# Kernel tuning notes

Measured on AMD Instinct MI355X. Metric: run time of the kernel, lower is better.

Reference implementation:

```python
import jax, jax.numpy as jnp
import numpy as np

B, S, D_IN, UNITS = 4, 4096, 256, 64


def setup_inputs() -> dict:
    key = jax.random.key(0)
    ks = jax.random.split(key, 4)
    scale = 1.0 / np.sqrt(D_IN)
    return {
        "x": jax.random.normal(ks[0], (B, S, D_IN), dtype=jnp.float32),
        "Wq": jax.random.normal(ks[1], (D_IN, UNITS), dtype=jnp.float32) * scale,
        "bq": jnp.zeros((UNITS,), dtype=jnp.float32),
        "Wk": jax.random.normal(ks[2], (D_IN, UNITS), dtype=jnp.float32) * scale,
        "bk": jnp.zeros((UNITS,), dtype=jnp.float32),
        "Wv": jax.random.normal(ks[3], (D_IN, UNITS), dtype=jnp.float32) * scale,
        "bv": jnp.zeros((UNITS,), dtype=jnp.float32),
    }


def reference(x, Wq, bq, Wk, bk, Wv, bv):
    # Q/K/V projections: [B, S, D_IN] @ [D_IN, UNITS] -> [B, S, UNITS]
    q = jnp.einsum("bsd,du->bsu", x, Wq) + bq
    k = jnp.einsum("bsd,du->bsu", x, Wk) + bk
    v = jnp.einsum("bsd,du->bsu", x, Wv) + bv
    # Full [B, S, S] scores (the module materializes these - headroom target)
    sims = jnp.einsum("bsu,btu->bst", q, k) / np.sqrt(UNITS).astype(np.float32)
    attn = jax.nn.softmax(sims, axis=-1)
    out = jnp.einsum("bst,btu->bsu", attn, v)
    return out  # activation is None (linear)
```

## Files before the change

### kernel.cpp

```cpp
#include <hip/hip_runtime.h>
#include <hip/hip_bf16.h>

#define B_ 4
#define S_ 4096
#define D_ 256
#define U_ 64
#define NROWS (B_ * S_)
#define QSCALE 0.1803368801111244f

typedef __attribute__((ext_vector_type(8))) short short8;
typedef __attribute__((ext_vector_type(8))) float float8;
typedef __attribute__((ext_vector_type(4))) float floatx4;

__device__ inline short f2bf(float f) {
    union { __hip_bfloat16 h; short s; } u;
    u.h = __float2bfloat16(f);
    return u.s;
}
__device__ inline unsigned pk2bf(float a, float b) {
    unsigned ua = __float_as_uint(a) + 0x8000u;
    unsigned ub = __float_as_uint(b) + 0x8000u;
    return (ub & 0xFFFF0000u) | (ua >> 16);
}

__global__ void pack_w_kernel(const float* __restrict__ Wq,
                              const float* __restrict__ Wk,
                              const float* __restrict__ Wv,
                              short* __restrict__ wpack) {
    int tid = blockIdx.x * 256 + threadIdx.x;
    if (tid >= 3 * 16384) return;
    int p = tid >> 14, e = tid & 16383;
    const float* W = (p == 0) ? Wq : (p == 1) ? Wk : Wv;
    float w = W[e];
    int k = e >> 6, n = e & 63;
    int ks = k >> 5, hi = (k >> 3) & 3, j = k & 7;
    int l = hi * 16 + (n & 15), nc = n >> 4;
    wpack[p * 16384 + ((ks * 4 + nc) * 64 + l) * 8 + j] = f2bf(w);
}

__global__ __launch_bounds__(256) void qkv_proj_kernel(
    const float* __restrict__ x, const short* __restrict__ wpack,
    const float* __restrict__ bq, const float* __restrict__ bk,
    const float* __restrict__ bv,
    short* __restrict__ Q, short* __restrict__ Kpack, short* __restrict__ Vpack) {
    __shared__ __align__(16) short k_sh[64][72];
    __shared__ __align__(16) short vT_sh[64][72];
    const int wl    = threadIdx.x >> 6;
    const int lane  = threadIdx.x & 63;
    const int col16 = lane & 15, quad = lane >> 4;
    const int m0b = blockIdx.x * 64, m0 = m0b + wl * 16;

    floatx4 acc[3][4];
#pragma unroll
    for (int p = 0; p < 3; ++p)
#pragma unroll
        for (int nc = 0; nc < 4; ++nc) acc[p][nc] = (floatx4){0.f, 0.f, 0.f, 0.f};

    const float* xrow = x + (size_t)(m0 + col16) * D_ + quad * 8;
#pragma unroll
    for (int ks = 0; ks < 8; ++ks) {
        float8 af = *(const float8*)(xrow + ks * 32);
        short8 a;
#pragma unroll
        for (int j = 0; j < 8; ++j) a[j] = f2bf(af[j]);
#pragma unroll
        for (int p = 0; p < 3; ++p) {
#pragma unroll
            for (int nc = 0; nc < 4; ++nc) {
                short8 bfr = *(const short8*)(wpack +
                    ((size_t)((p * 8 + ks) * 4 + nc) * 64 + lane) * 8);
                acc[p][nc] = __builtin_amdgcn_mfma_f32_16x16x32_bf16(a, bfr, acc[p][nc], 0, 0, 0);
            }
        }
    }

#pragma unroll
    for (int nc = 0; nc < 4; ++nc) {
        float biasq = bq[nc * 16 + col16];
        float biask = bk[nc * 16 + col16];
        float biasv = bv[nc * 16 + col16];
#pragma unroll
        for (int r = 0; r < 4; ++r) {
            int row = m0 + quad * 4 + r;
            Q[(size_t)row * U_ + nc * 16 + col16] = f2bf((acc[0][nc][r] + biasq) * QSCALE);
            k_sh[wl * 16 + quad * 4 + r][nc * 16 + col16] = f2bf(acc[1][nc][r] + biask);
        }
        union { short s[4]; unsigned long long u; } pv;
#pragma unroll
        for (int r = 0; r < 4; ++r) pv.s[r] = f2bf(acc[2][nc][r] + biasv);
        *(unsigned long long*)&vT_sh[nc * 16 + col16][wl * 16 + quad * 4] = pv.u;
    }
    __syncthreads();

#pragma unroll
    for (int c2 = 0; c2 < 2; ++c2) {
        int combo = wl + c2 * 4;
        int ww = combo >> 2, t = (combo >> 1) & 1, h = combo & 1;
        int srow = ww * 32 + (col16 >> 2) * 8 + (col16 & 3) + 4 * t;
        short8 v = *(const short8*)&k_sh[srow][h * 32 + quad * 8];
        size_t gt = (size_t)blockIdx.x * 2 + ww;
        *(short8*)(Kpack + (gt * 4 + t * 2 + h) * 512 + lane * 8) = v;
    }
#pragma unroll
    for (int c2 = 0; c2 < 2; ++c2) {
        int combo = wl + c2 * 4;
        int ww = combo >> 2, nc = combo & 3;
        short8 v = *(const short8*)&vT_sh[nc * 16 + col16][ww * 32 + quad * 8];
        size_t gt = (size_t)blockIdx.x * 2 + ww;
        *(short8*)(Vpack + (gt * 4 + nc) * 512 + lane * 8) = v;
    }
}

__global__ __launch_bounds__(512) void attn_kernel(
    const short* __restrict__ Q, const short* __restrict__ Kpack,
    const short* __restrict__ Vpack, float* __restrict__ out) {
    __shared__ float o_sh[2][64][65];
    __shared__ float l_sh[8][4][16];

    const int b  = blockIdx.y;
    const int q0 = blockIdx.x * 64;
    const int kw = threadIdx.x >> 6;
    const int lane  = threadIdx.x & 63;
    const int col16 = lane & 15, quad = lane >> 4;

    const short* Qb = Q + (size_t)b * S_ * U_;

    short8 bQ[4][2];
#pragma unroll
    for (int qs = 0; qs < 4; ++qs) {
        const short* qrow = Qb + (size_t)(q0 + qs * 16 + col16) * U_ + quad * 8;
        bQ[qs][0] = *(const short8*)(qrow);
        bQ[qs][1] = *(const short8*)(qrow + 32);
    }

    floatx4 o[4][4];
#pragma unroll
    for (int qs = 0; qs < 4; ++qs)
#pragma unroll
        for (int nc = 0; nc < 4; ++nc) o[qs][nc] = (floatx4){0.f, 0.f, 0.f, 0.f};
    float l_i[4] = {0.f, 0.f, 0.f, 0.f};

    const short* kbase = Kpack + ((size_t)(b * 128 + kw * 16)) * 2048 + lane * 8;
    const short* vbase = Vpack + ((size_t)(b * 128 + kw * 16)) * 2048 + lane * 8;

    for (int it = 0; it < 16; ++it) {
        const short* kp = kbase + it * 2048;
        const short* vp = vbase + it * 2048;
        short8 ak[2][2];
#pragma unroll
        for (int t = 0; t < 2; ++t)
#pragma unroll
            for (int h = 0; h < 2; ++h)
                ak[t][h] = *(const short8*)(kp + (t * 2 + h) * 512);
        short8 av[4];
#pragma unroll
        for (int nc = 0; nc < 4; ++nc)
            av[nc] = *(const short8*)(vp + nc * 512);

#pragma unroll
        for (int qs = 0; qs < 4; ++qs) {
            floatx4 c[2];
#pragma unroll
            for (int t = 0; t < 2; ++t) {
                c[t] = __builtin_amdgcn_mfma_f32_16x16x32_bf16(ak[t][0], bQ[qs][0],
                          (floatx4){0.f, 0.f, 0.f, 0.f}, 0, 0, 0);
                c[t] = __builtin_amdgcn_mfma_f32_16x16x32_bf16(ak[t][1], bQ[qs][1], c[t], 0, 0, 0);
            }
            float p[8];
            float rs = 0.f;
#pragma unroll
            for (int t = 0; t < 2; ++t)
#pragma unroll
                for (int r = 0; r < 4; ++r) {
                    float e = exp2f(c[t][r]);
                    p[t * 4 + r] = e;
                    rs += e;
                }
            l_i[qs] += rs;
            union { short8 s; unsigned u[4]; } pb;
            pb.u[0] = pk2bf(p[0], p[1]);
            pb.u[1] = pk2bf(p[2], p[3]);
            pb.u[2] = pk2bf(p[4], p[5]);
            pb.u[3] = pk2bf(p[6], p[7]);
#pragma unroll
            for (int nc = 0; nc < 4; ++nc)
                o[qs][nc] = __builtin_amdgcn_mfma_f32_16x16x32_bf16(av[nc], pb.s, o[qs][nc], 0, 0, 0);
        }
    }

#pragma unroll
    for (int qs = 0; qs < 4; ++qs) {
        l_i[qs] += __shfl_xor(l_i[qs], 16, 64);
        l_i[qs] += __shfl_xor(l_i[qs], 32, 64);
    }
    if (quad == 0) {
#pragma unroll
        for (int qs = 0; qs < 4; ++qs) l_sh[kw][qs][col16] = l_i[qs];
    }

    if (kw < 2) {
#pragma unroll
        for (int qs = 0; qs < 4; ++qs)
#pragma unroll
            for (int nc = 0; nc < 4; ++nc)
#pragma unroll
                for (int r = 0; r < 4; ++r)
                    o_sh[kw][qs * 16 + col16][nc * 16 + quad * 4 + r] = o[qs][nc][r];
    }
    __syncthreads();
    if (kw == 2 || kw == 3) {
#pragma unroll
        for (int qs = 0; qs < 4; ++qs)
#pragma unroll
            for (int nc = 0; nc < 4; ++nc)
#pragma unroll
                for (int r = 0; r < 4; ++r)
                    o_sh[kw - 2][qs * 16 + col16][nc * 16 + quad * 4 + r] += o[qs][nc][r];
    }
    __syncthreads();
    if (kw == 4 || kw == 5) {
#pragma unroll
        for (int qs = 0; qs < 4; ++qs)
#pragma unroll
            for (int nc = 0; nc < 4; ++nc)
#pragma unroll
                for (int r = 0; r < 4; ++r)
                    o_sh[kw - 4][qs * 16 + col16][nc * 16 + quad * 4 + r] += o[qs][nc][r];
    }
    __syncthreads();
    if (kw >= 6) {
#pragma unroll
        for (int qs = 0; qs < 4; ++qs)
#pragma unroll
            for (int nc = 0; nc < 4; ++nc)
#pragma unroll
                for (int r = 0; r < 4; ++r)
                    o_sh[kw - 6][qs * 16 + col16][nc * 16 + quad * 4 + r] += o[qs][nc][r];
    }
    __syncthreads();
    for (int i = threadIdx.x; i < 64 * 64; i += 512) {
        int row = i >> 6, col = i & 63;
        int qs2 = row >> 4, c = row & 15;
        float lt = 0.f;
#pragma unroll
        for (int ww = 0; ww < 8; ++ww) lt += l_sh[ww][qs2][c];
        float s = o_sh[0][row][col] + o_sh[1][row][col];
        out[((size_t)b * S_ + q0 + row) * U_ + col] = s / lt;
    }
}

extern "C" void kernel_launch(void* const* d_in, const int* in_sizes, int n_in,
                              void* d_out, int out_size, void* d_ws, size_t ws_size,
                              hipStream_t stream) {
    const float* x  = (const float*)d_in[0];
    const float* Wq = (const float*)d_in[1];
    const float* bq = (const float*)d_in[2];
    const float* Wk = (const float*)d_in[3];
    const float* bk = (const float*)d_in[4];
    const float* Wv = (const float*)d_in[5];
    const float* bv = (const float*)d_in[6];
    float* out = (float*)d_out;

    short* Q     = (short*)d_ws;
    short* Kpack = Q + (size_t)NROWS * U_;
    short* Vpack = Kpack + (size_t)NROWS * U_;
    short* wpack = Vpack + (size_t)NROWS * U_;

    pack_w_kernel<<<192, 256, 0, stream>>>(Wq, Wk, Wv, wpack);
    qkv_proj_kernel<<<NROWS / 64, 256, 0, stream>>>(
        x, wpack, bq, bk, bv, Q, Kpack, Vpack);
    attn_kernel<<<dim3(S_ / 64, B_), 512, 0, stream>>>(Q, Kpack, Vpack, out);
}
```

Baseline: 120.7 us.

## Double-buffer K/V tile loads, use native exp2, and swizzle block order

The attention loop now prefetches the next K/V tile into a second register buffer while computing the current one, so global-load latency overlaps with MFMA and exp work. exp2f is replaced by the hardware exp2 builtin when the compiler provides it. The launch becomes a 1D grid of 256 blocks whose index is remapped so that neighbouring blocks handle different batches, which is meant to spread K/V reads of one batch across XCDs or caches. The extra buffer raises VGPR pressure, which could hurt occupancy at 512 threads.

```diff
diff --git a/kernel.cpp b/kernel.cpp
--- a/kernel.cpp
+++ b/kernel.cpp
@@ -21,6 +21,13 @@
     unsigned ua = __float_as_uint(a) + 0x8000u;
     unsigned ub = __float_as_uint(b) + 0x8000u;
     return (ub & 0xFFFF0000u) | (ua >> 16);
+}
+__device__ inline float fast_exp2(float x) {
+#if __has_builtin(__builtin_amdgcn_exp2f)
+    return __builtin_amdgcn_exp2f(x);
+#else
+    return exp2f(x);
+#endif
 }
 
 __global__ void pack_w_kernel(const float* __restrict__ Wq,
@@ -111,14 +118,64 @@
     }
 }
 
+#define LOAD_TILE(bi, off)                                                   \
+    do {                                                                     \
+        const short* kp_ = kbase + (off) * 2048;                             \
+        const short* vp_ = vbase + (off) * 2048;                             \
+        _Pragma("unroll")                                                    \
+        for (int t = 0; t < 2; ++t)                                          \
+            _Pragma("unroll")                                                \
+            for (int h = 0; h < 2; ++h)                                      \
+                ak[bi][t][h] = *(const short8*)(kp_ + (t * 2 + h) * 512);    \
+        _Pragma("unroll")                                                    \
+        for (int nc = 0; nc < 4; ++nc)                                       \
+            av[bi][nc] = *(const short8*)(vp_ + nc * 512);                   \
+    } while (0)
+
+#define COMPUTE_TILE(bi)                                                                   \
+    do {                                                                                   \
+        _Pragma("unroll")                                                                  \
+        for (int qs = 0; qs < 4; ++qs) {                                                   \
+            floatx4 c[2];                                                                  \
+            _Pragma("unroll")                                                              \
+            for (int t = 0; t < 2; ++t) {                                                  \
+                c[t] = __builtin_amdgcn_mfma_f32_16x16x32_bf16(ak[bi][t][0], bQ[qs][0],    \
+                          (floatx4){0.f, 0.f, 0.f, 0.f}, 0, 0, 0);                         \
+                c[t] = __builtin_amdgcn_mfma_f32_16x16x32_bf16(ak[bi][t][1], bQ[qs][1],    \
+                          c[t], 0, 0, 0);                                                  \
+            }                                                                              \
+            float p[8];                                                                    \
+            float rs = 0.f;                                                                \
+            _Pragma("unroll")                                                              \
+            for (int t = 0; t < 2; ++t)                                                    \
+                _Pragma("unroll")                                                          \
+                for (int r = 0; r < 4; ++r) {                                              \
+                    float e = fast_exp2(c[t][r]);                                          \
+                    p[t * 4 + r] = e;                                                      \
+                    rs += e;                                                               \
+                }                                                                          \
+            l_i[qs] += rs;                                                                 \
+            union { short8 s; unsigned u[4]; } pb;                                         \
+            pb.u[0] = pk2bf(p[0], p[1]);                                                   \
+            pb.u[1] = pk2bf(p[2], p[3]);                                                   \
+            pb.u[2] = pk2bf(p[4], p[5]);                                                   \
+            pb.u[3] = pk2bf(p[6], p[7]);                                                   \
+            _Pragma("unroll")                                                              \
+            for (int nc = 0; nc < 4; ++nc)                                                 \
+                o[qs][nc] = __builtin_amdgcn_mfma_f32_16x16x32_bf16(av[bi][nc], pb.s,      \
+                                o[qs][nc], 0, 0, 0);                                       \
+        }                                                                                  \
+    } while (0)
+
 __global__ __launch_bounds__(512) void attn_kernel(
     const short* __restrict__ Q, const short* __restrict__ Kpack,
     const short* __restrict__ Vpack, float* __restrict__ out) {
     __shared__ float o_sh[2][64][65];
     __shared__ float l_sh[8][4][16];
 
-    const int b  = blockIdx.y;
-    const int q0 = blockIdx.x * 64;
+    const int i  = blockIdx.x;
+    const int b  = (i & 7) >> 1;
+    const int q0 = ((((i >> 3) << 1) | (i & 1))) * 64;
     const int kw = threadIdx.x >> 6;
     const int lane  = threadIdx.x & 63;
     const int col16 = lane & 15, quad = lane >> 4;
@@ -143,49 +200,13 @@
     const short* kbase = Kpack + ((size_t)(b * 128 + kw * 16)) * 2048 + lane * 8;
     const short* vbase = Vpack + ((size_t)(b * 128 + kw * 16)) * 2048 + lane * 8;
 
-    for (int it = 0; it < 16; ++it) {
-        const short* kp = kbase + it * 2048;
-        const short* vp = vbase + it * 2048;
-        short8 ak[2][2];
-#pragma unroll
-        for (int t = 0; t < 2; ++t)
-#pragma unroll
-            for (int h = 0; h < 2; ++h)
-                ak[t][h] = *(const short8*)(kp + (t * 2 + h) * 512);
-        short8 av[4];
-#pragma unroll
-        for (int nc = 0; nc < 4; ++nc)
-            av[nc] = *(const short8*)(vp + nc * 512);
-
-#pragma unroll
-        for (int qs = 0; qs < 4; ++qs) {
-            floatx4 c[2];
-#pragma unroll
-            for (int t = 0; t < 2; ++t) {
-                c[t] = __builtin_amdgcn_mfma_f32_16x16x32_bf16(ak[t][0], bQ[qs][0],
-                          (floatx4){0.f, 0.f, 0.f, 0.f}, 0, 0, 0);
-                c[t] = __builtin_amdgcn_mfma_f32_16x16x32_bf16(ak[t][1], bQ[qs][1], c[t], 0, 0, 0);
-            }
-            float p[8];
-            float rs = 0.f;
-#pragma unroll
-            for (int t = 0; t < 2; ++t)
-#pragma unroll
-                for (int r = 0; r < 4; ++r) {
-                    float e = exp2f(c[t][r]);
-                    p[t * 4 + r] = e;
-                    rs += e;
-                }
-            l_i[qs] += rs;
-            union { short8 s; unsigned u[4]; } pb;
-            pb.u[0] = pk2bf(p[0], p[1]);
-            pb.u[1] = pk2bf(p[2], p[3]);
-            pb.u[2] = pk2bf(p[4], p[5]);
-            pb.u[3] = pk2bf(p[6], p[7]);
-#pragma unroll
-            for (int nc = 0; nc < 4; ++nc)
-                o[qs][nc] = __builtin_amdgcn_mfma_f32_16x16x32_bf16(av[nc], pb.s, o[qs][nc], 0, 0, 0);
-        }
+    short8 ak[2][2][2], av[2][4];
+    LOAD_TILE(0, 0);
+    for (int it = 0; it < 16; it += 2) {
+        LOAD_TILE(1, it + 1);
+        COMPUTE_TILE(0);
+        if (it + 2 < 16) LOAD_TILE(0, it + 2);
+        COMPUTE_TILE(1);
     }
 
 #pragma unroll
@@ -238,8 +259,8 @@
                     o_sh[kw - 6][qs * 16 + col16][nc * 16 + quad * 4 + r] += o[qs][nc][r];
     }
     __syncthreads();
-    for (int i = threadIdx.x; i < 64 * 64; i += 512) {
-        int row = i >> 6, col = i & 63;
+    for (int i2 = threadIdx.x; i2 < 64 * 64; i2 += 512) {
+        int row = i2 >> 6, col = i2 & 63;
         int qs2 = row >> 4, c = row & 15;
         float lt = 0.f;
 #pragma unroll
@@ -269,5 +290,5 @@
     pack_w_kernel<<<192, 256, 0, stream>>>(Wq, Wk, Wv, wpack);
     qkv_proj_kernel<<<NROWS / 64, 256, 0, stream>>>(
         x, wpack, bq, bk, bv, Q, Kpack, Vpack);
-    attn_kernel<<<dim3(S_ / 64, B_), 512, 0, stream>>>(Q, Kpack, Vpack, out);
-}
+    attn_kernel<<<256, 512, 0, stream>>>(Q, Kpack, Vpack, out);
+}
```

Result: faster. 107.7 us (-10.8%).
